# Performance work log

Measured on AMD Instinct MI355X. Metric: run time of the kernel, lower is better.

The kernel has to match this reference:

```python
import jax, jax.numpy as jnp
import numpy as np

NUM_HEADS = 12   # H
NUM_TASKS = 4    # T
TOP_K = 2        # capacity_factor


def setup_inputs() -> dict:
    key = jax.random.key(0)
    ks = jax.random.split(key, 4)
    B, N, C = 2, 4100, 768  # N = NUM_TASKS + M, M = 4096
    x = jax.random.normal(ks[0], (B, N, C), dtype=jnp.float32)
    # torch.nn.Linear weights are [out_features, in_features]; y = x @ W.T
    qs_w = jax.random.normal(ks[1], (NUM_TASKS, C, C), dtype=jnp.float32) * 0.02
    kv_w = jax.random.normal(ks[2], (2 * C, C), dtype=jnp.float32) * 0.02
    experts_w = jax.random.normal(ks[3], (NUM_TASKS, C, C), dtype=jnp.float32) * 0.02
    return {"x": x, "qs_w": qs_w, "kv_w": kv_w, "experts_w": experts_w}


def reference(x, qs_w, kv_w, experts_w):
    B, N, C = x.shape
    T, H, K = NUM_TASKS, NUM_HEADS, TOP_K
    d = C // H
    M = N - T
    scale = d ** -0.5

    feature = x[:, T:, :]                                    # [B,M,C]
    kv = (feature @ kv_w.T).reshape(B, M, 2, H, d)
    k = jnp.transpose(kv[:, :, 0], (0, 2, 1, 3))             # [B,H,M,d]
    v = jnp.transpose(kv[:, :, 1], (0, 2, 1, 3))             # [B,H,M,d]

    # per-task q projections on task tokens (qs_w[t] is [out,in])
    q = jnp.einsum('btc,toc->bto', x[:, :T], qs_w)           # [B,T,C]
    q = q.reshape(B, T, H, d).transpose(0, 2, 1, 3)          # [B,H,T,d]

    attn = jnp.einsum('bhtd,bhmd->bhtm', q, k) * scale       # [B,H,T,M]
    topv, topi = jax.lax.top_k(attn, K)                      # [B,H,T,K]
    topw = jax.nn.softmax(topv, axis=-1)                     # softmax over top-k only

    # scatter softmaxed top-k back into dense [B,H,T,M] (indices unique per row)
    oh = jax.nn.one_hot(topi, M, dtype=x.dtype)              # [B,H,T,K,M]
    attn_topk = jnp.einsum('bhtk,bhtkm->bhtm', topw, oh)
    attn_token = jnp.einsum('bhtm,bhmd->bhtd', attn_topk, v)
    attn_token = attn_token.transpose(0, 2, 1, 3).reshape(B, T, C)   # [B,T,C]

    # gather top-k feature rows per head/task, weight, and scatter back
    fm = feature.reshape(B, M, H, d).transpose(0, 2, 1, 3)   # [B,H,M,d]
    feat_topk = jnp.take_along_axis(fm[:, :, None], topi[..., None], axis=3)  # [B,H,T,K,d]
    feat_topk = feat_topk * topw[..., None]
    # scatter to [B,H,T,M,d], then permute(0,2,3,1,4)+reshape -> [B,T,M,C]
    feat_pad = jnp.einsum('bhtkd,bhtkm->btmhd', feat_topk, oh).reshape(B, T, M, C)

    # per-task experts (no bias); einsum('btnc,btnc->bnc') with ones = sum over t
    feature_output = jnp.einsum('btmc,toc->bmo', feat_pad, experts_w)  # [B,M,C]
    token_output = jnp.einsum('btc,toc->bto', attn_token, experts_w)   # [B,T,C]

    return jnp.concatenate([token_output, feature_output], axis=1)     # [B,N,C]
```

## Files before the change

### kernel.cpp

```cpp
#include <hip/hip_runtime.h>
#include <math.h>

#define B_ 2
#define N_ 4100
#define C_ 768
#define T_ 4
#define H_ 12
#define D_ 64
#define M_ 4096
#define S_ 48
#define KS_ 12
#define KC_ 64
#define SEG_ 8
#define SCALE 0.125f

__device__ __forceinline__ bool better(float va, int ia, float vb, int ib) {
  return (va > vb) || (va == vb && ia < ib);
}

__device__ __forceinline__ void merge2(float& v1, int& i1, float& v2, int& i2,
                                       float ov1, int oi1, float ov2, int oi2) {
  if (better(ov1, oi1, v1, i1)) {
    float tv; int ti;
    tv = v1; ti = i1; v1 = ov1; i1 = oi1; ov1 = tv; oi1 = ti;
    tv = v2; ti = i2; v2 = ov2; i2 = oi2; ov2 = tv; oi2 = ti;
  }
  if (better(ov1, oi1, v2, i2)) { v2 = ov1; i2 = oi1; }
}

__global__ __launch_bounds__(256) void qk_kernel(const float* __restrict__ x,
    const float* __restrict__ qs_w, const float* __restrict__ kv_w,
    float* __restrict__ qk, float* __restrict__ out) {
  const int h = blockIdx.x % H_;
  const int t = (blockIdx.x / H_) % T_;
  const int b = blockIdx.x / S_;
  const int tid = threadIdx.x;
  __shared__ float xs[C_];
  __shared__ float red[256];
  __shared__ float qseg[D_];
  if (h == 0)
    for (int i = tid; i < C_; i += 256) out[((size_t)b * N_ + t) * C_ + i] = 0.f;
  for (int i = tid; i < C_; i += 256) xs[i] = x[((size_t)b * N_ + t) * C_ + i];
  __syncthreads();
  {
    const int j = tid & 63;
    const int pt = tid >> 6;
    const float* wr = qs_w + ((size_t)t * C_ + h * D_ + j) * C_ + pt * 192;
    float a = 0.f;
    for (int c = 0; c < 192; ++c) a += xs[pt * 192 + c] * wr[c];
    red[tid] = a;
  }
  __syncthreads();
  if (tid < 64)
    qseg[tid] = (red[tid] + red[tid + 64] + red[tid + 128] + red[tid + 192]) * SCALE;
  __syncthreads();
  for (int c = tid; c < C_; c += 256) {
    float a = 0.f;
    #pragma unroll 8
    for (int j = 0; j < 64; ++j) a += qseg[j] * kv_w[((size_t)(h * D_ + j)) * C_ + c];
    qk[((size_t)blockIdx.x) * C_ + c] = a;
  }
}

__global__ __launch_bounds__(256) void score_kernel(const float* __restrict__ x,
    const float* __restrict__ qk, float* __restrict__ part, float* __restrict__ out) {
  const int mt = blockIdx.x & 63;
  const int b = blockIdx.x >> 6;
  const int kc = blockIdx.y;
  const int tid = threadIdx.x;
  const int m0 = mt * 64;

  __shared__ __align__(16) float fbuf[64][68];
  __shared__ __align__(16) float qkbuf[48][68];

  if (kc == 0) {
    float4 z = make_float4(0.f, 0.f, 0.f, 0.f);
    float4* outv = (float4*)(out + ((size_t)b * N_ + T_ + m0) * C_);
    for (int i = tid; i < 64 * C_ / 4; i += 256) outv[i] = z;
  }

  const float* xb = x + ((size_t)b * N_ + T_ + m0) * C_ + kc * KC_;
  const float* qkb = qk + (size_t)b * S_ * C_ + kc * KC_;

  for (int i = tid; i < 64 * 16; i += 256) {
    int row = i >> 4, c4 = i & 15;
    *(float4*)&fbuf[row][c4 * 4] =
        *(const float4*)(xb + (size_t)row * C_ + c4 * 4);
  }
  for (int i = tid; i < 48 * 16; i += 256) {
    int s = i >> 4, c4 = i & 15;
    *(float4*)&qkbuf[s][c4 * 4] =
        *(const float4*)(qkb + (size_t)s * C_ + c4 * 4);
  }
  __syncthreads();

  const int mg = tid & 15;
  const int sg = tid >> 4;

  float acc[4][3];
  #pragma unroll
  for (int u = 0; u < 4; ++u)
    #pragma unroll
    for (int i = 0; i < 3; ++i) acc[u][i] = 0.f;

  #pragma unroll 4
  for (int c4 = 0; c4 < 16; ++c4) {
    float4 f[4], q[3];
    f[0] = *(const float4*)&fbuf[mg][c4 * 4];
    f[1] = *(const float4*)&fbuf[mg + 16][c4 * 4];
    f[2] = *(const float4*)&fbuf[mg + 32][c4 * 4];
    f[3] = *(const float4*)&fbuf[mg + 48][c4 * 4];
    q[0] = *(const float4*)&qkbuf[sg * 3 + 0][c4 * 4];
    q[1] = *(const float4*)&qkbuf[sg * 3 + 1][c4 * 4];
    q[2] = *(const float4*)&qkbuf[sg * 3 + 2][c4 * 4];
    #pragma unroll
    for (int u = 0; u < 4; ++u)
      #pragma unroll
      for (int i = 0; i < 3; ++i)
        acc[u][i] += f[u].x * q[i].x + f[u].y * q[i].y +
                     f[u].z * q[i].z + f[u].w * q[i].w;
  }

  #pragma unroll
  for (int i = 0; i < 3; ++i) {
    int s = sg * 3 + i;
    float* pp = part + (((size_t)kc * B_ + b) * S_ + s) * M_ + m0 + mg;
    #pragma unroll
    for (int u = 0; u < 4; ++u) pp[16 * u] = acc[u][i];
  }
}

__global__ __launch_bounds__(256) void reduce_kernel(const float* __restrict__ part,
                                                     float* __restrict__ cand) {
  const int seg = blockIdx.x & 7;
  const int bs = blockIdx.x >> 3;
  const int tid = threadIdx.x;
  const size_t kstride = (size_t)B_ * S_ * M_;
  const float* p0 = part + (size_t)bs * M_ + seg * 512 + tid * 2;
  float a0 = 0.f, a1 = 0.f;
  #pragma unroll
  for (int kc = 0; kc < KS_; ++kc) {
    float2 v = *(const float2*)(p0 + kc * kstride);
    a0 += v.x; a1 += v.y;
  }
  const int mA = seg * 512 + tid * 2;
  float v1, v2; int i1, i2;
  if (better(a0, mA, a1, mA + 1)) { v1 = a0; i1 = mA; v2 = a1; i2 = mA + 1; }
  else                            { v1 = a1; i1 = mA + 1; v2 = a0; i2 = mA; }
  #pragma unroll
  for (int off = 1; off < 64; off <<= 1) {
    float ov1 = __shfl_xor(v1, off);
    int   oi1 = __shfl_xor(i1, off);
    float ov2 = __shfl_xor(v2, off);
    int   oi2 = __shfl_xor(i2, off);
    merge2(v1, i1, v2, i2, ov1, oi1, ov2, oi2);
  }
  __shared__ float cbuf[4][4];
  const int w = tid >> 6, lane = tid & 63;
  if (lane == 0) {
    cbuf[w][0] = v1; ((int*)cbuf[w])[1] = i1;
    cbuf[w][2] = v2; ((int*)cbuf[w])[3] = i2;
  }
  __syncthreads();
  if (tid == 0) {
    for (int ww = 1; ww < 4; ++ww)
      merge2(v1, i1, v2, i2, cbuf[ww][0], ((int*)cbuf[ww])[1],
             cbuf[ww][2], ((int*)cbuf[ww])[3]);
    ((float4*)cand)[blockIdx.x] =
        make_float4(v1, __int_as_float(i1), v2, __int_as_float(i2));
  }
}

__global__ __launch_bounds__(256) void gather_kernel(const float* __restrict__ x,
    const float* __restrict__ kv_w, const float* __restrict__ experts_w,
    const float* __restrict__ cand, float* __restrict__ out) {
  const int h = blockIdx.x % H_;
  const int t = (blockIdx.x / H_) % T_;
  const int b = blockIdx.x / S_;
  const int tid = threadIdx.x;

  __shared__ float f0[C_], f1[C_], fc[C_], red[256];
  __shared__ float attnh[D_];
  __shared__ float sel[4];

  if (tid < 8) {
    float4 cv = ((const float4*)cand)[blockIdx.x * 8 + tid];
    float v1 = cv.x, v2 = cv.z;
    int i1 = __float_as_int(cv.y), i2 = __float_as_int(cv.w);
    #pragma unroll
    for (int off = 1; off < 8; off <<= 1) {
      float ov1 = __shfl_xor(v1, off);
      int   oi1 = __shfl_xor(i1, off);
      float ov2 = __shfl_xor(v2, off);
      int   oi2 = __shfl_xor(i2, off);
      merge2(v1, i1, v2, i2, ov1, oi1, ov2, oi2);
    }
    if (tid == 0) {
      float w1 = 1.f / (1.f + expf(v2 - v1));
      ((int*)sel)[0] = i1; ((int*)sel)[1] = i2;
      sel[2] = w1; sel[3] = 1.f - w1;
    }
  }
  __syncthreads();
  const int i1 = ((const int*)sel)[0];
  const int i2 = ((const int*)sel)[1];
  const float w1 = sel[2], w2 = sel[3];

  const float* r0 = x + ((size_t)b * N_ + T_ + i1) * C_;
  const float* r1 = x + ((size_t)b * N_ + T_ + i2) * C_;
  for (int i = tid; i < C_; i += 256) {
    float a = r0[i], bb = r1[i];
    f0[i] = a; f1[i] = bb; fc[i] = w1 * a + w2 * bb;
  }
  __syncthreads();

  const int j = tid & 63, pt = tid >> 6;
  {
    const float* kr = kv_w + ((size_t)(C_ + h * D_ + j)) * C_ + pt * 192;
    float a = 0.f;
    for (int c = 0; c < 192; ++c) a += fc[pt * 192 + c] * kr[c];
    red[tid] = a;
  }
  __syncthreads();
  if (tid < 64)
    attnh[tid] = red[tid] + red[tid + 64] + red[tid + 128] + red[tid + 192];
  __syncthreads();

  const size_t ot = ((size_t)b * N_ + t) * C_;
  const size_t o0 = ((size_t)b * N_ + T_ + i1) * C_;
  const size_t o1 = ((size_t)b * N_ + T_ + i2) * C_;
  for (int o = tid; o < C_; o += 256) {
    const float* er = experts_w + ((size_t)t * C_ + o) * C_ + h * D_;
    float at = 0.f, a0 = 0.f, a1 = 0.f;
    #pragma unroll 8
    for (int c = 0; c < D_; ++c) {
      float e = er[c];
      at += e * attnh[c];
      a0 += e * f0[h * D_ + c];
      a1 += e * f1[h * D_ + c];
    }
    atomicAdd(&out[ot + o], at);
    atomicAdd(&out[o0 + o], w1 * a0);
    atomicAdd(&out[o1 + o], w2 * a1);
  }
}

extern "C" void kernel_launch(void* const* d_in, const int* in_sizes, int n_in,
                              void* d_out, int out_size, void* d_ws, size_t ws_size,
                              hipStream_t stream) {
  const float* x         = (const float*)d_in[0];
  const float* qs_w      = (const float*)d_in[1];
  const float* kv_w      = (const float*)d_in[2];
  const float* experts_w = (const float*)d_in[3];
  float* out = (float*)d_out;

  float* ws   = (float*)d_ws;
  float* qk   = ws;
  float* part = qk + (size_t)B_ * S_ * C_;
  float* cand = part + (size_t)KS_ * B_ * S_ * M_;

  hipLaunchKernelGGL(qk_kernel,     dim3(B_ * S_),        dim3(256), 0, stream, x, qs_w, kv_w, qk, out);
  hipLaunchKernelGGL(score_kernel,  dim3(B_ * 64, KS_),   dim3(256), 0, stream, x, qk, part, out);
  hipLaunchKernelGGL(reduce_kernel, dim3(B_ * S_ * SEG_), dim3(256), 0, stream, part, cand);
  hipLaunchKernelGGL(gather_kernel, dim3(B_ * S_),        dim3(256), 0, stream, x, kv_w, experts_w, cand, out);
}
```

Before: 149.7 us.

## Move output zeroing into the qk kernel and halve the split-K partial count

Output zeroing moves out of the score kernel into extra blocks of the qk kernel. Those blocks clear the whole output with float4 stores while the 96 qk blocks compute the projections. The score kernel's split-K factor drops from 12 to 6, and each block now loops over two 64-wide channel chunks in shared memory. This halves the partial-score buffer that the reduce kernel writes and reads. The cost is fewer score blocks with more serial work per block, plus an extra sync pair per chunk.

```diff
diff --git a/kernel.cpp b/kernel.cpp
--- a/kernel.cpp
+++ b/kernel.cpp
@@ -9,9 +9,10 @@
 #define D_ 64
 #define M_ 4096
 #define S_ 48
-#define KS_ 12
-#define KC_ 64
+#define KS_ 6
+#define KC_ 128
 #define SEG_ 8
+#define GRID_ 768
 #define SCALE 0.125f
 
 __device__ __forceinline__ bool better(float va, int ia, float vb, int ib) {
@@ -28,42 +29,49 @@
   if (better(ov1, oi1, v2, i2)) { v2 = ov1; i2 = oi1; }
 }
 
-__global__ __launch_bounds__(256) void qk_kernel(const float* __restrict__ x,
+__global__ __launch_bounds__(256) void qkzero_kernel(const float* __restrict__ x,
     const float* __restrict__ qs_w, const float* __restrict__ kv_w,
     float* __restrict__ qk, float* __restrict__ out) {
-  const int h = blockIdx.x % H_;
-  const int t = (blockIdx.x / H_) % T_;
-  const int b = blockIdx.x / S_;
-  const int tid = threadIdx.x;
-  __shared__ float xs[C_];
-  __shared__ float red[256];
-  __shared__ float qseg[D_];
-  if (h == 0)
-    for (int i = tid; i < C_; i += 256) out[((size_t)b * N_ + t) * C_ + i] = 0.f;
-  for (int i = tid; i < C_; i += 256) xs[i] = x[((size_t)b * N_ + t) * C_ + i];
-  __syncthreads();
-  {
-    const int j = tid & 63;
-    const int pt = tid >> 6;
-    const float* wr = qs_w + ((size_t)t * C_ + h * D_ + j) * C_ + pt * 192;
-    float a = 0.f;
-    for (int c = 0; c < 192; ++c) a += xs[pt * 192 + c] * wr[c];
-    red[tid] = a;
-  }
-  __syncthreads();
-  if (tid < 64)
-    qseg[tid] = (red[tid] + red[tid + 64] + red[tid + 128] + red[tid + 192]) * SCALE;
-  __syncthreads();
-  for (int c = tid; c < C_; c += 256) {
-    float a = 0.f;
-    #pragma unroll 8
-    for (int j = 0; j < 64; ++j) a += qseg[j] * kv_w[((size_t)(h * D_ + j)) * C_ + c];
-    qk[((size_t)blockIdx.x) * C_ + c] = a;
+  const int blk = blockIdx.x;
+  const int tid = threadIdx.x;
+  if (blk < B_ * S_) {
+    const int h = blk % H_;
+    const int t = (blk / H_) % T_;
+    const int b = blk / S_;
+    __shared__ float xs[C_];
+    __shared__ float red[256];
+    __shared__ float qseg[D_];
+    for (int i = tid; i < C_; i += 256) xs[i] = x[((size_t)b * N_ + t) * C_ + i];
+    __syncthreads();
+    {
+      const int j = tid & 63;
+      const int pt = tid >> 6;
+      const float* wr = qs_w + ((size_t)t * C_ + h * D_ + j) * C_ + pt * 192;
+      float a = 0.f;
+      for (int c = 0; c < 192; ++c) a += xs[pt * 192 + c] * wr[c];
+      red[tid] = a;
+    }
+    __syncthreads();
+    if (tid < 64)
+      qseg[tid] = (red[tid] + red[tid + 64] + red[tid + 128] + red[tid + 192]) * SCALE;
+    __syncthreads();
+    for (int c = tid; c < C_; c += 256) {
+      float a = 0.f;
+      #pragma unroll 8
+      for (int j = 0; j < 64; ++j) a += qseg[j] * kv_w[((size_t)(h * D_ + j)) * C_ + c];
+      qk[(size_t)blk * C_ + c] = a;
+    }
+  } else {
+    const int zb = blk - B_ * S_;
+    const int NV4 = (B_ * N_ * C_) / 4;
+    float4 z = make_float4(0.f, 0.f, 0.f, 0.f);
+    float4* ov = (float4*)out;
+    for (int i = zb * 256 + tid; i < NV4; i += (GRID_ - B_ * S_) * 256) ov[i] = z;
   }
 }
 
 __global__ __launch_bounds__(256) void score_kernel(const float* __restrict__ x,
-    const float* __restrict__ qk, float* __restrict__ part, float* __restrict__ out) {
+    const float* __restrict__ qk, float* __restrict__ part) {
   const int mt = blockIdx.x & 63;
   const int b = blockIdx.x >> 6;
   const int kc = blockIdx.y;
@@ -73,27 +81,6 @@
   __shared__ __align__(16) float fbuf[64][68];
   __shared__ __align__(16) float qkbuf[48][68];
 
-  if (kc == 0) {
-    float4 z = make_float4(0.f, 0.f, 0.f, 0.f);
-    float4* outv = (float4*)(out + ((size_t)b * N_ + T_ + m0) * C_);
-    for (int i = tid; i < 64 * C_ / 4; i += 256) outv[i] = z;
-  }
-
-  const float* xb = x + ((size_t)b * N_ + T_ + m0) * C_ + kc * KC_;
-  const float* qkb = qk + (size_t)b * S_ * C_ + kc * KC_;
-
-  for (int i = tid; i < 64 * 16; i += 256) {
-    int row = i >> 4, c4 = i & 15;
-    *(float4*)&fbuf[row][c4 * 4] =
-        *(const float4*)(xb + (size_t)row * C_ + c4 * 4);
-  }
-  for (int i = tid; i < 48 * 16; i += 256) {
-    int s = i >> 4, c4 = i & 15;
-    *(float4*)&qkbuf[s][c4 * 4] =
-        *(const float4*)(qkb + (size_t)s * C_ + c4 * 4);
-  }
-  __syncthreads();
-
   const int mg = tid & 15;
   const int sg = tid >> 4;
 
@@ -103,22 +90,39 @@
     #pragma unroll
     for (int i = 0; i < 3; ++i) acc[u][i] = 0.f;
 
-  #pragma unroll 4
-  for (int c4 = 0; c4 < 16; ++c4) {
-    float4 f[4], q[3];
-    f[0] = *(const float4*)&fbuf[mg][c4 * 4];
-    f[1] = *(const float4*)&fbuf[mg + 16][c4 * 4];
-    f[2] = *(const float4*)&fbuf[mg + 32][c4 * 4];
-    f[3] = *(const float4*)&fbuf[mg + 48][c4 * 4];
-    q[0] = *(const float4*)&qkbuf[sg * 3 + 0][c4 * 4];
-    q[1] = *(const float4*)&qkbuf[sg * 3 + 1][c4 * 4];
-    q[2] = *(const float4*)&qkbuf[sg * 3 + 2][c4 * 4];
-    #pragma unroll
-    for (int u = 0; u < 4; ++u)
+  const float* xb = x + ((size_t)b * N_ + T_ + m0) * C_ + kc * KC_;
+  const float* qkb = qk + (size_t)b * S_ * C_ + kc * KC_;
+
+  for (int cc = 0; cc < KC_ / 64; ++cc) {
+    __syncthreads();
+    for (int i = tid; i < 64 * 16; i += 256) {
+      int row = i >> 4, c4 = i & 15;
+      *(float4*)&fbuf[row][c4 * 4] =
+          *(const float4*)(xb + (size_t)row * C_ + cc * 64 + c4 * 4);
+    }
+    for (int i = tid; i < 48 * 16; i += 256) {
+      int s = i >> 4, c4 = i & 15;
+      *(float4*)&qkbuf[s][c4 * 4] =
+          *(const float4*)(qkb + (size_t)s * C_ + cc * 64 + c4 * 4);
+    }
+    __syncthreads();
+    #pragma unroll 4
+    for (int c4 = 0; c4 < 16; ++c4) {
+      float4 f[4], q[3];
+      f[0] = *(const float4*)&fbuf[mg][c4 * 4];
+      f[1] = *(const float4*)&fbuf[mg + 16][c4 * 4];
+      f[2] = *(const float4*)&fbuf[mg + 32][c4 * 4];
+      f[3] = *(const float4*)&fbuf[mg + 48][c4 * 4];
+      q[0] = *(const float4*)&qkbuf[sg * 3 + 0][c4 * 4];
+      q[1] = *(const float4*)&qkbuf[sg * 3 + 1][c4 * 4];
+      q[2] = *(const float4*)&qkbuf[sg * 3 + 2][c4 * 4];
       #pragma unroll
-      for (int i = 0; i < 3; ++i)
-        acc[u][i] += f[u].x * q[i].x + f[u].y * q[i].y +
-                     f[u].z * q[i].z + f[u].w * q[i].w;
+      for (int u = 0; u < 4; ++u)
+        #pragma unroll
+        for (int i = 0; i < 3; ++i)
+          acc[u][i] += f[u].x * q[i].x + f[u].y * q[i].y +
+                       f[u].z * q[i].z + f[u].w * q[i].w;
+    }
   }
 
   #pragma unroll
@@ -259,8 +263,8 @@
   float* part = qk + (size_t)B_ * S_ * C_;
   float* cand = part + (size_t)KS_ * B_ * S_ * M_;
 
-  hipLaunchKernelGGL(qk_kernel,     dim3(B_ * S_),        dim3(256), 0, stream, x, qs_w, kv_w, qk, out);
-  hipLaunchKernelGGL(score_kernel,  dim3(B_ * 64, KS_),   dim3(256), 0, stream, x, qk, part, out);
+  hipLaunchKernelGGL(qkzero_kernel, dim3(GRID_),          dim3(256), 0, stream, x, qs_w, kv_w, qk, out);
+  hipLaunchKernelGGL(score_kernel,  dim3(B_ * 64, KS_),   dim3(256), 0, stream, x, qk, part);
   hipLaunchKernelGGL(reduce_kernel, dim3(B_ * S_ * SEG_), dim3(256), 0, stream, part, cand);
   hipLaunchKernelGGL(gather_kernel, dim3(B_ * S_),        dim3(256), 0, stream, x, kv_w, experts_w, cand, out);
 }
```

Measured after the change: 144.4 us, median of 2. 1.04x faster.
